# Kernel tuning notes

Measured on AMD Instinct MI355X. Metric: run time of the kernel, lower is better.

## Reference

```python
import jax, jax.numpy as jnp
import numpy as np

N_NODES = 131072
N_EDGES = 4194304
NUM_GRAPHS = 128


def setup_inputs() -> dict:
    key = jax.random.key(0)
    ks = jax.random.split(key, 12)
    x = jax.random.normal(ks[0], (N_NODES, 3), dtype=jnp.float32)
    edge_index = jax.random.randint(ks[1], (2, N_EDGES), 0, N_NODES, dtype=jnp.int32)
    batch = jnp.sort(jax.random.randint(ks[2], (N_NODES,), 0, NUM_GRAPHS, dtype=jnp.int32))
    W1 = jax.random.normal(ks[3], (3, 16), dtype=jnp.float32) * 0.5
    b1 = jax.random.normal(ks[4], (16,), dtype=jnp.float32) * 0.1
    W2 = jax.random.normal(ks[5], (16, 64), dtype=jnp.float32) * 0.25
    b2 = jax.random.normal(ks[6], (64,), dtype=jnp.float32) * 0.1
    fcw1 = jax.random.normal(ks[7], (64, 32), dtype=jnp.float32) * 0.125
    fcb1 = jax.random.normal(ks[8], (32,), dtype=jnp.float32) * 0.1
    fcw2 = jax.random.normal(ks[9], (32, 2), dtype=jnp.float32) * 0.2
    fcb2 = jax.random.normal(ks[10], (2,), dtype=jnp.float32) * 0.1
    return dict(x=x, edge_index=edge_index, batch=batch, W1=W1, b1=b1,
                W2=W2, b2=b2, fcw1=fcw1, fcb1=fcb1, fcw2=fcw2, fcb2=fcb2)


def _gcn_conv(x, W, b, src, dst, n_nodes):
    # PyG GCNConv: add self-loops, symmetric D^-1/2 A_hat D^-1/2, then scatter-add at dst.
    h = x @ W  # [N, out]
    deg = jax.ops.segment_sum(jnp.ones_like(dst, dtype=h.dtype), dst, num_segments=n_nodes)
    dinv = jnp.where(deg > 0, jax.lax.rsqrt(jnp.maximum(deg, 1.0)), 0.0)
    norm = dinv[src] * dinv[dst]  # [E]
    msgs = norm[:, None] * h[src]  # gather + scale, [E, out]
    return jax.ops.segment_sum(msgs, dst, num_segments=n_nodes) + b


def reference(x, edge_index, batch, W1, b1, W2, b2, fcw1, fcb1, fcw2, fcb2):
    n = x.shape[0]
    loop = jnp.arange(n, dtype=edge_index.dtype)
    src = jnp.concatenate([edge_index[0], loop])
    dst = jnp.concatenate([edge_index[1], loop])
    h = jax.nn.relu(_gcn_conv(x, W1, b1, src, dst, n))
    h = jax.nn.relu(_gcn_conv(h, W2, b2, src, dst, n))
    # global_mean_pool over batch ids
    s = jax.ops.segment_sum(h, batch, num_segments=NUM_GRAPHS)
    cnt = jax.ops.segment_sum(jnp.ones((n,), h.dtype), batch, num_segments=NUM_GRAPHS)
    g = s / jnp.maximum(cnt, 1.0)[:, None]  # [G, 64]
    g = g @ fcw1 + fcb1
    return g @ fcw2 + fcb2  # [G, 2]
```

## Files before the change

kernel.cpp:

```cpp
#include <hip/hip_runtime.h>
#include <hip/hip_fp16.h>

#define N_NODES 131072
#define N_EDGES 4194304
#define NUM_GRAPHS 128

#define NB 512
#define NPB 256
#define BSHIFT 8
#define BCAP 10240
#define GSPAN 8

typedef int iv4 __attribute__((ext_vector_type(4)));

__device__ __forceinline__ int scan256(int tid, int v, int* wsum) {
  __syncthreads();
  int incl = v;
  #pragma unroll
  for (int d = 1; d < 64; d <<= 1) {
    int t = __shfl_up(incl, d);
    if ((tid & 63) >= d) incl += t;
  }
  if (tid < NPB && (tid & 63) == 63) wsum[tid >> 6] = incl;
  __syncthreads();
  int base = 0;
  int wv = tid >> 6;
  #pragma unroll
  for (int w2 = 0; w2 < 4; ++w2)
    if (w2 < wv) base += wsum[w2];
  return base + incl - v;
}

__global__ __launch_bounds__(1024) void k_binfill(const iv4* __restrict__ src4,
                                                  const iv4* __restrict__ dst4,
                                                  int* __restrict__ bcount,
                                                  unsigned* __restrict__ binned) {
  __shared__ int hist[NB], base_[NB], rank_[NB];
  for (int k = threadIdx.x; k < NB; k += 1024) { hist[k] = 0; rank_[k] = 0; }
  __syncthreads();
  unsigned pk[16];
  int bk[16];
  int q0 = blockIdx.x * 4096 + threadIdx.x;
  #pragma unroll
  for (int i = 0; i < 4; ++i) {
    iv4 sv = __builtin_nontemporal_load(&src4[q0 + i * 1024]);
    iv4 dv = __builtin_nontemporal_load(&dst4[q0 + i * 1024]);
    #pragma unroll
    for (int j = 0; j < 4; ++j) {
      int idx = i * 4 + j;
      int s = sv[j], d = dv[j];
      bk[idx] = d >> BSHIFT;
      pk[idx] = ((unsigned)s << BSHIFT) | (unsigned)(d & (NPB - 1));
      atomicAdd(&hist[bk[idx]], 1);
    }
  }
  __syncthreads();
  for (int k = threadIdx.x; k < NB; k += 1024)
    base_[k] = k * BCAP + atomicAdd(&bcount[k], hist[k]);
  __syncthreads();
  #pragma unroll
  for (int i = 0; i < 16; ++i) {
    int r = atomicAdd(&rank_[bk[i]], 1);
    binned[base_[bk[i]] + r] = pk[i];
  }
}

__global__ __launch_bounds__(1024) void k_prep(const unsigned* __restrict__ binned,
                                               const int* __restrict__ bcount,
                                               const float* __restrict__ x,
                                               float* __restrict__ dinv,
                                               float4* __restrict__ xs4) {
  __shared__ int dcount[NPB];
  int tid = threadIdx.x;
  if (tid < NPB) dcount[tid] = 0;
  __syncthreads();
  int b = blockIdx.x;
  int s0 = b * BCAP;
  int n = bcount[b];
  for (int e = tid; e < n; e += 1024) {
    unsigned ent = __builtin_nontemporal_load(&binned[s0 + e]);
    atomicAdd(&dcount[ent & (NPB - 1)], 1);
  }
  __syncthreads();
  if (tid < NPB) {
    int node = b * NPB + tid;
    float di = rsqrtf((float)(dcount[tid] + 1));
    dinv[node] = di;
    xs4[node] = make_float4(di * x[node * 3 + 0], di * x[node * 3 + 1],
                            di * x[node * 3 + 2], 0.f);
  }
}

__global__ __launch_bounds__(1024) void k_sagg3h1(const unsigned* __restrict__ binned,
                                                  const int* __restrict__ bcount,
                                                  const float* __restrict__ xs,
                                                  const float4* __restrict__ xs4,
                                                  const float* __restrict__ dinv,
                                                  const float* __restrict__ W1,
                                                  const float* __restrict__ b1,
                                                  unsigned* __restrict__ h1h) {
  __shared__ int dcount[NPB], cursor[NPB], nbase[NPB], perm[NPB];
  __shared__ int wsum[4];
  __shared__ int csrL[BCAP];
  __shared__ float w[48];
  __shared__ float bb[16];
  __shared__ float accS[NPB * 4];
  int tid = threadIdx.x;
  if (tid >= 512 && tid < 560) w[tid - 512] = W1[tid - 512];
  if (tid >= 576 && tid < 592) bb[tid - 576] = b1[tid - 576];
  if (tid < NPB) dcount[tid] = 0;
  __syncthreads();

  int b = blockIdx.x;
  int s0 = b * BCAP;
  int n = bcount[b];
  unsigned ent_r[10];
  #pragma unroll
  for (int j = 0; j < 10; ++j) {
    int e = tid + j * 1024;
    if (e < n) {
      unsigned ent = __builtin_nontemporal_load(&binned[s0 + e]);
      ent_r[j] = ent;
      atomicAdd(&dcount[ent & (NPB - 1)], 1);
    }
  }
  __syncthreads();

  int v = (tid < NPB) ? dcount[tid] : 0;
  int pref = scan256(tid, v, wsum);
  if (tid < NPB) { cursor[tid] = pref; nbase[tid] = pref; }
  __syncthreads();

  #pragma unroll
  for (int j = 0; j < 10; ++j) {
    int e = tid + j * 1024;
    if (e < n) {
      unsigned ent = ent_r[j];
      int pos = atomicAdd(&cursor[ent & (NPB - 1)], 1);
      csrL[pos] = (int)(ent >> BSHIFT) << 4;
    }
  }

  __syncthreads();
  if (tid < NPB) cursor[tid] = 0;
  __syncthreads();
  int key = (tid < NPB) ? min(v, NPB - 1) : 0;
  if (tid < NPB) atomicAdd(&cursor[key], 1);
  __syncthreads();
  int dv2 = (tid < NPB) ? cursor[tid] : 0;
  int dpref = scan256(tid, dv2, wsum);
  __syncthreads();
  if (tid < NPB) cursor[tid] = dpref;
  __syncthreads();
  if (tid < NPB) {
    int r = atomicAdd(&cursor[key], 1);
    perm[r] = tid;
  }
  __syncthreads();

  int dl = perm[tid >> 2];
  int q = tid & 3;
  int off = nbase[dl];
  int len = dcount[dl];
  const char* xsc = (const char*)xs;
  int qb = q << 2;
  float acc = 0.f;
  #pragma unroll 4
  for (int k = 0; k < len; ++k) {
    int bo = csrL[off + k];
    acc += *(const float*)(xsc + bo + qb);
  }
  accS[dl * 4 + q] = acc;
  __syncthreads();

  int dle = tid >> 2;
  int qe = tid & 3;
  int node = b * NPB + dle;
  float di = dinv[node];
  float4 xself = xs4[node];
  float a0 = di * (accS[dle * 4 + 0] + xself.x);
  float a1 = di * (accS[dle * 4 + 1] + xself.y);
  float a2 = di * (accS[dle * 4 + 2] + xself.z);
  float o[4];
  #pragma unroll
  for (int j = 0; j < 4; ++j) {
    int cc = qe * 4 + j;
    float vv = a0 * w[cc] + a1 * w[16 + cc] + a2 * w[32 + cc] + bb[cc];
    o[j] = di * fmaxf(vv, 0.f);
  }
  __half2 p0 = __floats2half2_rn(o[0], o[1]);
  __half2 p1 = __floats2half2_rn(o[2], o[3]);
  uint2 st;
  st.x = *reinterpret_cast<unsigned*>(&p0);
  st.y = *reinterpret_cast<unsigned*>(&p1);
  *(uint2*)(h1h + (size_t)node * 8 + qe * 2) = st;
}

__global__ __launch_bounds__(1024) void k_sagg16pool(const unsigned* __restrict__ binned,
                                                     const int* __restrict__ bcount,
                                                     const unsigned* __restrict__ h1h,
                                                     const float* __restrict__ dinv,
                                                     const int* __restrict__ batch,
                                                     const float* __restrict__ W2,
                                                     const float* __restrict__ b2,
                                                     float* __restrict__ gsum) {
  __shared__ int dcount[NPB], cursor[NPB], nbase[NPB], perm[NPB];
  __shared__ int wsum[4];
  __shared__ int csrL[BCAP];
  __shared__ float aggS[NPB * 16];
  __shared__ float w2s[1024];
  __shared__ float b2s[64];
  __shared__ float gacc[GSPAN * 64];
  int tid = threadIdx.x;
  w2s[tid] = W2[tid];
  if (tid < 64) b2s[tid] = b2[tid];
  if (tid < GSPAN * 64) gacc[tid] = 0.f;
  if (tid < NPB) dcount[tid] = 0;
  __syncthreads();

  int b = blockIdx.x;
  int s0 = b * BCAP;
  int n = bcount[b];
  unsigned ent_r[10];
  #pragma unroll
  for (int j = 0; j < 10; ++j) {
    int e = tid + j * 1024;
    if (e < n) {
      unsigned ent = __builtin_nontemporal_load(&binned[s0 + e]);
      ent_r[j] = ent;
      atomicAdd(&dcount[ent & (NPB - 1)], 1);
    }
  }
  __syncthreads();

  int v = (tid < NPB) ? dcount[tid] : 0;
  int pref = scan256(tid, v, wsum);
  if (tid < NPB) { cursor[tid] = pref; nbase[tid] = pref; }
  __syncthreads();

  #pragma unroll
  for (int j = 0; j < 10; ++j) {
    int e = tid + j * 1024;
    if (e < n) {
      unsigned ent = ent_r[j];
      int pos = atomicAdd(&cursor[ent & (NPB - 1)], 1);
      csrL[pos] = (int)(ent >> BSHIFT) << 5;
    }
  }

  __syncthreads();
  if (tid < NPB) cursor[tid] = 0;
  __syncthreads();
  int key = (tid < NPB) ? min(v, NPB - 1) : 0;
  if (tid < NPB) atomicAdd(&cursor[key], 1);
  __syncthreads();
  int dv2 = (tid < NPB) ? cursor[tid] : 0;
  int dpref = scan256(tid, dv2, wsum);
  __syncthreads();
  if (tid < NPB) cursor[tid] = dpref;
  __syncthreads();
  if (tid < NPB) {
    int r = atomicAdd(&cursor[key], 1);
    perm[r] = tid;
  }
  __syncthreads();

  const char* h1c = (const char*)h1h;
  int dl = perm[tid >> 2];
  int q = tid & 3;
  int qb = q << 3;
  int node = b * NPB + dl;
  int off = nbase[dl];
  int len = dcount[dl];
  float o0 = 0.f, o1 = 0.f, o2 = 0.f, o3 = 0.f;
  #pragma unroll 4
  for (int k = 0; k < len; ++k) {
    int bo = csrL[off + k];
    uint2 hv = *(const uint2*)(h1c + bo + qb);
    __half2 p0 = *reinterpret_cast<const __half2*>(&hv.x);
    __half2 p1 = *reinterpret_cast<const __half2*>(&hv.y);
    o0 += __low2float(p0); o1 += __high2float(p0);
    o2 += __low2float(p1); o3 += __high2float(p1);
  }
  float di = dinv[node];
  uint2 sv = *(const uint2*)(h1h + (size_t)node * 8 + q * 2);
  __half2 s0h = *reinterpret_cast<const __half2*>(&sv.x);
  __half2 s1h = *reinterpret_cast<const __half2*>(&sv.y);
  aggS[dl * 16 + q * 4 + 0] = di * (o0 + __low2float(s0h));
  aggS[dl * 16 + q * 4 + 1] = di * (o1 + __high2float(s0h));
  aggS[dl * 16 + q * 4 + 2] = di * (o2 + __low2float(s1h));
  aggS[dl * 16 + q * 4 + 3] = di * (o3 + __high2float(s1h));
  __syncthreads();

  int c = tid & 63;
  int slot = tid >> 6;
  int g0 = batch[b * NPB];
  float racc = 0.f;
  int curli = -1;
  for (int nloc = slot; nloc < NPB; nloc += 16) {
    int nd = b * NPB + nloc;
    int li = batch[nd] - g0;
    if (li != curli) {
      if (curli >= 0) {
        if (curli < GSPAN) atomicAdd(&gacc[curli * 64 + c], racc);
        else atomicAdd(&gsum[(size_t)(g0 + curli) * 64 + c], racc);
      }
      curli = li;
      racc = 0.f;
    }
    float vv = b2s[c];
    const float* ar = &aggS[nloc * 16];
    #pragma unroll
    for (int k = 0; k < 16; ++k) vv += ar[k] * w2s[k * 64 + c];
    racc += fmaxf(vv, 0.f);
  }
  if (curli >= 0) {
    if (curli < GSPAN) atomicAdd(&gacc[curli * 64 + c], racc);
    else atomicAdd(&gsum[(size_t)(g0 + curli) * 64 + c], racc);
  }
  __syncthreads();

  int span = batch[b * NPB + NPB - 1] - g0 + 1;
  if (span > GSPAN) span = GSPAN;
  for (int li = tid >> 6; li < span; li += 16) {
    atomicAdd(&gsum[(size_t)(g0 + li) * 64 + c], gacc[li * 64 + c]);
  }
}

__global__ __launch_bounds__(64) void k_fc(const float* __restrict__ gsum,
                                           const int* __restrict__ batch,
                                           const float* __restrict__ fcw1,
                                           const float* __restrict__ fcb1,
                                           const float* __restrict__ fcw2,
                                           const float* __restrict__ fcb2,
                                           float* __restrict__ out) {
  int g = blockIdx.x;
  int lo = 0, hi = N_NODES;
  while (lo < hi) { int m = (lo + hi) >> 1; if (batch[m] < g) lo = m + 1; else hi = m; }
  int start = lo;
  lo = start; hi = N_NODES;
  while (lo < hi) { int m = (lo + hi) >> 1; if (batch[m] < g + 1) lo = m + 1; else hi = m; }
  float inv = 1.0f / fmaxf((float)(lo - start), 1.0f);

  __shared__ float gmean[64];
  gmean[threadIdx.x] = gsum[(size_t)g * 64 + threadIdx.x] * inv;
  __syncthreads();

  __shared__ float hid[32];
  if (threadIdx.x < 32) {
    float a = fcb1[threadIdx.x];
    #pragma unroll
    for (int k = 0; k < 64; ++k) a += gmean[k] * fcw1[k * 32 + threadIdx.x];
    hid[threadIdx.x] = a;
  }
  __syncthreads();

  if (threadIdx.x < 2) {
    float a = fcb2[threadIdx.x];
    #pragma unroll
    for (int k = 0; k < 32; ++k) a += hid[k] * fcw2[k * 2 + threadIdx.x];
    out[g * 2 + threadIdx.x] = a;
  }
}

extern "C" void kernel_launch(void* const* d_in, const int* in_sizes, int n_in,
                              void* d_out, int out_size, void* d_ws, size_t ws_size,
                              hipStream_t stream) {
  const float* x    = (const float*)d_in[0];
  const int*   ei   = (const int*)d_in[1];
  const int*   batch= (const int*)d_in[2];
  const float* W1   = (const float*)d_in[3];
  const float* b1   = (const float*)d_in[4];
  const float* W2   = (const float*)d_in[5];
  const float* b2   = (const float*)d_in[6];
  const float* fcw1 = (const float*)d_in[7];
  const float* fcb1 = (const float*)d_in[8];
  const float* fcw2 = (const float*)d_in[9];
  const float* fcb2 = (const float*)d_in[10];
  float* out = (float*)d_out;

  char* w = (char*)d_ws;
  size_t off = 0;
  auto alloc = [&](size_t bytes) {
    void* p = w + off;
    off += (bytes + 255) & ~(size_t)255;
    return p;
  };
  float*    gsum    = (float*)   alloc((size_t)NUM_GRAPHS * 64 * 4);
  int*      bcount  = (int*)     alloc((size_t)NB * 4);
  unsigned* binned  = (unsigned*)alloc((size_t)NB * BCAP * 4);
  float*    dinv    = (float*)   alloc((size_t)N_NODES * 4);
  float4*   xs4     = (float4*)  alloc((size_t)N_NODES * 16);
  unsigned* h1h     = (unsigned*)alloc((size_t)N_NODES * 32);

  const iv4* src4 = (const iv4*)ei;
  const iv4* dst4 = (const iv4*)(ei + N_EDGES);

  (void)hipMemsetAsync(gsum, 0, (size_t)NUM_GRAPHS * 64 * 4 + (size_t)NB * 4, stream);
  k_binfill<<<N_EDGES / 16384, 1024, 0, stream>>>(src4, dst4, bcount, binned);
  k_prep<<<NB, 1024, 0, stream>>>(binned, bcount, x, dinv, xs4);
  k_sagg3h1<<<NB, 1024, 0, stream>>>(binned, bcount, (const float*)xs4, xs4, dinv, W1, b1, h1h);
  k_sagg16pool<<<NB, 1024, 0, stream>>>(binned, bcount, h1h, dinv, batch, W2, b2, gsum);
  k_fc<<<NUM_GRAPHS, 64, 0, stream>>>(gsum, batch, fcw1, fcb1, fcw2, fcb2, out);
}
```

Before: 120.7 us.

## Halve destination bin size, drop degree-sort permutation, single-pass binfill ranks

Bins now hold 128 destination nodes instead of 256, giving 1024 blocks of 512 threads for the three per-bin kernels, with bin capacity and the scan resized to match. The degree-sorted permutation (a second histogram, scan and scatter with several barriers) is removed, so each thread group handles its node in natural order. k_binfill now takes per-edge ranks from the same shared atomic that builds the histogram, which removes a second atomic pass. The aim is better occupancy and less synchronisation, at the cost of more load imbalance between lanes inside a wavefront, and of bin overflow if any bin exceeds 5120 edges.

```diff
diff --git a/kernel.cpp b/kernel.cpp
--- a/kernel.cpp
+++ b/kernel.cpp
@@ -5,15 +5,15 @@
 #define N_EDGES 4194304
 #define NUM_GRAPHS 128
 
-#define NB 512
-#define NPB 256
-#define BSHIFT 8
-#define BCAP 10240
+#define NB 1024
+#define NPB 128
+#define BSHIFT 7
+#define BCAP 5120
 #define GSPAN 8
 
 typedef int iv4 __attribute__((ext_vector_type(4)));
 
-__device__ __forceinline__ int scan256(int tid, int v, int* wsum) {
+__device__ __forceinline__ int scan128(int tid, int v, int* wsum) {
   __syncthreads();
   int incl = v;
   #pragma unroll
@@ -23,11 +23,7 @@
   }
   if (tid < NPB && (tid & 63) == 63) wsum[tid >> 6] = incl;
   __syncthreads();
-  int base = 0;
-  int wv = tid >> 6;
-  #pragma unroll
-  for (int w2 = 0; w2 < 4; ++w2)
-    if (w2 < wv) base += wsum[w2];
+  int base = (tid >= 64 && tid < NPB) ? wsum[0] : 0;
   return base + incl - v;
 }
 
@@ -35,11 +31,11 @@
                                                   const iv4* __restrict__ dst4,
                                                   int* __restrict__ bcount,
                                                   unsigned* __restrict__ binned) {
-  __shared__ int hist[NB], base_[NB], rank_[NB];
-  for (int k = threadIdx.x; k < NB; k += 1024) { hist[k] = 0; rank_[k] = 0; }
+  __shared__ int base_[NB], rank_[NB];
+  for (int k = threadIdx.x; k < NB; k += 1024) rank_[k] = 0;
   __syncthreads();
   unsigned pk[16];
-  int bk[16];
+  int bk[16], rr[16];
   int q0 = blockIdx.x * 4096 + threadIdx.x;
   #pragma unroll
   for (int i = 0; i < 4; ++i) {
@@ -51,25 +47,23 @@
       int s = sv[j], d = dv[j];
       bk[idx] = d >> BSHIFT;
       pk[idx] = ((unsigned)s << BSHIFT) | (unsigned)(d & (NPB - 1));
-      atomicAdd(&hist[bk[idx]], 1);
+      rr[idx] = atomicAdd(&rank_[bk[idx]], 1);
     }
   }
   __syncthreads();
   for (int k = threadIdx.x; k < NB; k += 1024)
-    base_[k] = k * BCAP + atomicAdd(&bcount[k], hist[k]);
-  __syncthreads();
-  #pragma unroll
-  for (int i = 0; i < 16; ++i) {
-    int r = atomicAdd(&rank_[bk[i]], 1);
-    binned[base_[bk[i]] + r] = pk[i];
-  }
-}
-
-__global__ __launch_bounds__(1024) void k_prep(const unsigned* __restrict__ binned,
-                                               const int* __restrict__ bcount,
-                                               const float* __restrict__ x,
-                                               float* __restrict__ dinv,
-                                               float4* __restrict__ xs4) {
+    base_[k] = k * BCAP + atomicAdd(&bcount[k], rank_[k]);
+  __syncthreads();
+  #pragma unroll
+  for (int i = 0; i < 16; ++i)
+    binned[base_[bk[i]] + rr[i]] = pk[i];
+}
+
+__global__ __launch_bounds__(512) void k_prep(const unsigned* __restrict__ binned,
+                                              const int* __restrict__ bcount,
+                                              const float* __restrict__ x,
+                                              float* __restrict__ dinv,
+                                              float4* __restrict__ xs4) {
   __shared__ int dcount[NPB];
   int tid = threadIdx.x;
   if (tid < NPB) dcount[tid] = 0;
@@ -77,7 +71,7 @@
   int b = blockIdx.x;
   int s0 = b * BCAP;
   int n = bcount[b];
-  for (int e = tid; e < n; e += 1024) {
+  for (int e = tid; e < n; e += 512) {
     unsigned ent = __builtin_nontemporal_load(&binned[s0 + e]);
     atomicAdd(&dcount[ent & (NPB - 1)], 1);
   }
@@ -91,23 +85,23 @@
   }
 }
 
-__global__ __launch_bounds__(1024) void k_sagg3h1(const unsigned* __restrict__ binned,
-                                                  const int* __restrict__ bcount,
-                                                  const float* __restrict__ xs,
-                                                  const float4* __restrict__ xs4,
-                                                  const float* __restrict__ dinv,
-                                                  const float* __restrict__ W1,
-                                                  const float* __restrict__ b1,
-                                                  unsigned* __restrict__ h1h) {
-  __shared__ int dcount[NPB], cursor[NPB], nbase[NPB], perm[NPB];
-  __shared__ int wsum[4];
+__global__ __launch_bounds__(512) void k_sagg3h1(const unsigned* __restrict__ binned,
+                                                 const int* __restrict__ bcount,
+                                                 const float* __restrict__ xs,
+                                                 const float4* __restrict__ xs4,
+                                                 const float* __restrict__ dinv,
+                                                 const float* __restrict__ W1,
+                                                 const float* __restrict__ b1,
+                                                 unsigned* __restrict__ h1h) {
+  __shared__ int dcount[NPB], cursor[NPB], nbase[NPB];
+  __shared__ int wsum[2];
   __shared__ int csrL[BCAP];
   __shared__ float w[48];
   __shared__ float bb[16];
   __shared__ float accS[NPB * 4];
   int tid = threadIdx.x;
-  if (tid >= 512 && tid < 560) w[tid - 512] = W1[tid - 512];
-  if (tid >= 576 && tid < 592) bb[tid - 576] = b1[tid - 576];
+  if (tid >= 256 && tid < 304) w[tid - 256] = W1[tid - 256];
+  if (tid >= 320 && tid < 336) bb[tid - 320] = b1[tid - 320];
   if (tid < NPB) dcount[tid] = 0;
   __syncthreads();
 
@@ -117,7 +111,7 @@
   unsigned ent_r[10];
   #pragma unroll
   for (int j = 0; j < 10; ++j) {
-    int e = tid + j * 1024;
+    int e = tid + j * 512;
     if (e < n) {
       unsigned ent = __builtin_nontemporal_load(&binned[s0 + e]);
       ent_r[j] = ent;
@@ -127,39 +121,24 @@
   __syncthreads();
 
   int v = (tid < NPB) ? dcount[tid] : 0;
-  int pref = scan256(tid, v, wsum);
+  int pref = scan128(tid, v, wsum);
   if (tid < NPB) { cursor[tid] = pref; nbase[tid] = pref; }
   __syncthreads();
 
   #pragma unroll
   for (int j = 0; j < 10; ++j) {
-    int e = tid + j * 1024;
+    int e = tid + j * 512;
     if (e < n) {
       unsigned ent = ent_r[j];
       int pos = atomicAdd(&cursor[ent & (NPB - 1)], 1);
       csrL[pos] = (int)(ent >> BSHIFT) << 4;
     }
   }
-
-  __syncthreads();
-  if (tid < NPB) cursor[tid] = 0;
-  __syncthreads();
-  int key = (tid < NPB) ? min(v, NPB - 1) : 0;
-  if (tid < NPB) atomicAdd(&cursor[key], 1);
-  __syncthreads();
-  int dv2 = (tid < NPB) ? cursor[tid] : 0;
-  int dpref = scan256(tid, dv2, wsum);
-  __syncthreads();
-  if (tid < NPB) cursor[tid] = dpref;
-  __syncthreads();
-  if (tid < NPB) {
-    int r = atomicAdd(&cursor[key], 1);
-    perm[r] = tid;
-  }
-  __syncthreads();
-
-  int dl = perm[tid >> 2];
+  __syncthreads();
+
+  int dl = tid >> 2;
   int q = tid & 3;
+  int node = b * NPB + dl;
   int off = nbase[dl];
   int len = dcount[dl];
   const char* xsc = (const char*)xs;
@@ -170,21 +149,18 @@
     int bo = csrL[off + k];
     acc += *(const float*)(xsc + bo + qb);
   }
-  accS[dl * 4 + q] = acc;
-  __syncthreads();
-
-  int dle = tid >> 2;
-  int qe = tid & 3;
-  int node = b * NPB + dle;
+  accS[tid] = acc;
+  __syncthreads();
+
   float di = dinv[node];
   float4 xself = xs4[node];
-  float a0 = di * (accS[dle * 4 + 0] + xself.x);
-  float a1 = di * (accS[dle * 4 + 1] + xself.y);
-  float a2 = di * (accS[dle * 4 + 2] + xself.z);
+  float a0 = di * (accS[dl * 4 + 0] + xself.x);
+  float a1 = di * (accS[dl * 4 + 1] + xself.y);
+  float a2 = di * (accS[dl * 4 + 2] + xself.z);
   float o[4];
   #pragma unroll
   for (int j = 0; j < 4; ++j) {
-    int cc = qe * 4 + j;
+    int cc = q * 4 + j;
     float vv = a0 * w[cc] + a1 * w[16 + cc] + a2 * w[32 + cc] + bb[cc];
     o[j] = di * fmaxf(vv, 0.f);
   }
@@ -193,19 +169,19 @@
   uint2 st;
   st.x = *reinterpret_cast<unsigned*>(&p0);
   st.y = *reinterpret_cast<unsigned*>(&p1);
-  *(uint2*)(h1h + (size_t)node * 8 + qe * 2) = st;
-}
-
-__global__ __launch_bounds__(1024) void k_sagg16pool(const unsigned* __restrict__ binned,
-                                                     const int* __restrict__ bcount,
-                                                     const unsigned* __restrict__ h1h,
-                                                     const float* __restrict__ dinv,
-                                                     const int* __restrict__ batch,
-                                                     const float* __restrict__ W2,
-                                                     const float* __restrict__ b2,
-                                                     float* __restrict__ gsum) {
-  __shared__ int dcount[NPB], cursor[NPB], nbase[NPB], perm[NPB];
-  __shared__ int wsum[4];
+  *(uint2*)(h1h + (size_t)node * 8 + q * 2) = st;
+}
+
+__global__ __launch_bounds__(512) void k_sagg16pool(const unsigned* __restrict__ binned,
+                                                    const int* __restrict__ bcount,
+                                                    const unsigned* __restrict__ h1h,
+                                                    const float* __restrict__ dinv,
+                                                    const int* __restrict__ batch,
+                                                    const float* __restrict__ W2,
+                                                    const float* __restrict__ b2,
+                                                    float* __restrict__ gsum) {
+  __shared__ int dcount[NPB], cursor[NPB], nbase[NPB];
+  __shared__ int wsum[2];
   __shared__ int csrL[BCAP];
   __shared__ float aggS[NPB * 16];
   __shared__ float w2s[1024];
@@ -213,6 +189,7 @@
   __shared__ float gacc[GSPAN * 64];
   int tid = threadIdx.x;
   w2s[tid] = W2[tid];
+  w2s[tid + 512] = W2[tid + 512];
   if (tid < 64) b2s[tid] = b2[tid];
   if (tid < GSPAN * 64) gacc[tid] = 0.f;
   if (tid < NPB) dcount[tid] = 0;
@@ -224,7 +201,7 @@
   unsigned ent_r[10];
   #pragma unroll
   for (int j = 0; j < 10; ++j) {
-    int e = tid + j * 1024;
+    int e = tid + j * 512;
     if (e < n) {
       unsigned ent = __builtin_nontemporal_load(&binned[s0 + e]);
       ent_r[j] = ent;
@@ -234,39 +211,23 @@
   __syncthreads();
 
   int v = (tid < NPB) ? dcount[tid] : 0;
-  int pref = scan256(tid, v, wsum);
+  int pref = scan128(tid, v, wsum);
   if (tid < NPB) { cursor[tid] = pref; nbase[tid] = pref; }
   __syncthreads();
 
   #pragma unroll
   for (int j = 0; j < 10; ++j) {
-    int e = tid + j * 1024;
+    int e = tid + j * 512;
     if (e < n) {
       unsigned ent = ent_r[j];
       int pos = atomicAdd(&cursor[ent & (NPB - 1)], 1);
       csrL[pos] = (int)(ent >> BSHIFT) << 5;
     }
   }
-
-  __syncthreads();
-  if (tid < NPB) cursor[tid] = 0;
-  __syncthreads();
-  int key = (tid < NPB) ? min(v, NPB - 1) : 0;
-  if (tid < NPB) atomicAdd(&cursor[key], 1);
-  __syncthreads();
-  int dv2 = (tid < NPB) ? cursor[tid] : 0;
-  int dpref = scan256(tid, dv2, wsum);
-  __syncthreads();
-  if (tid < NPB) cursor[tid] = dpref;
-  __syncthreads();
-  if (tid < NPB) {
-    int r = atomicAdd(&cursor[key], 1);
-    perm[r] = tid;
-  }
   __syncthreads();
 
   const char* h1c = (const char*)h1h;
-  int dl = perm[tid >> 2];
+  int dl = tid >> 2;
   int q = tid & 3;
   int qb = q << 3;
   int node = b * NPB + dl;
@@ -297,7 +258,7 @@
   int g0 = batch[b * NPB];
   float racc = 0.f;
   int curli = -1;
-  for (int nloc = slot; nloc < NPB; nloc += 16) {
+  for (int nloc = slot; nloc < NPB; nloc += 8) {
     int nd = b * NPB + nloc;
     int li = batch[nd] - g0;
     if (li != curli) {
@@ -322,7 +283,7 @@
 
   int span = batch[b * NPB + NPB - 1] - g0 + 1;
   if (span > GSPAN) span = GSPAN;
-  for (int li = tid >> 6; li < span; li += 16) {
+  for (int li = tid >> 6; li < span; li += 8) {
     atomicAdd(&gsum[(size_t)(g0 + li) * 64 + c], gacc[li * 64 + c]);
   }
 }
@@ -398,8 +359,8 @@
 
   (void)hipMemsetAsync(gsum, 0, (size_t)NUM_GRAPHS * 64 * 4 + (size_t)NB * 4, stream);
   k_binfill<<<N_EDGES / 16384, 1024, 0, stream>>>(src4, dst4, bcount, binned);
-  k_prep<<<NB, 1024, 0, stream>>>(binned, bcount, x, dinv, xs4);
-  k_sagg3h1<<<NB, 1024, 0, stream>>>(binned, bcount, (const float*)xs4, xs4, dinv, W1, b1, h1h);
-  k_sagg16pool<<<NB, 1024, 0, stream>>>(binned, bcount, h1h, dinv, batch, W2, b2, gsum);
+  k_prep<<<NB, 512, 0, stream>>>(binned, bcount, x, dinv, xs4);
+  k_sagg3h1<<<NB, 512, 0, stream>>>(binned, bcount, (const float*)xs4, xs4, dinv, W1, b1, h1h);
+  k_sagg16pool<<<NB, 512, 0, stream>>>(binned, bcount, h1h, dinv, batch, W2, b2, gsum);
   k_fc<<<NUM_GRAPHS, 64, 0, stream>>>(gsum, batch, fcw1, fcb1, fcw2, fcb2, out);
 }
```

Result: slower. 135.0 us (+11.8%).
